# Performance work log

Hardware: AMD Instinct MI355X
Metric: run time of the kernel (lower is better)

## Reference

```python
import jax, jax.numpy as jnp
import numpy as np

B, T, I, H, O, L = 64, 1024, 128, 512, 64, 3


def setup_inputs() -> dict:
    key = jax.random.key(0)
    ks = jax.random.split(key, 16)
    s = 1.0 / np.sqrt(H)  # PyTorch RNN init scale U(-1/sqrt(H), 1/sqrt(H)); use scaled normal
    d = {
        "x": jax.random.normal(ks[0], (B, T, I), jnp.float32),
        "h0": jnp.zeros((L, B, H), jnp.float32),
        "w_ih0": jax.random.normal(ks[1], (H, I), jnp.float32) * s,
        "w_hh0": jax.random.normal(ks[2], (H, H), jnp.float32) * s,
        "b_ih0": jax.random.normal(ks[3], (H,), jnp.float32) * s,
        "b_hh0": jax.random.normal(ks[4], (H,), jnp.float32) * s,
        "w_ih1": jax.random.normal(ks[5], (H, H), jnp.float32) * s,
        "w_hh1": jax.random.normal(ks[6], (H, H), jnp.float32) * s,
        "b_ih1": jax.random.normal(ks[7], (H,), jnp.float32) * s,
        "b_hh1": jax.random.normal(ks[8], (H,), jnp.float32) * s,
        "w_ih2": jax.random.normal(ks[9], (H, H), jnp.float32) * s,
        "w_hh2": jax.random.normal(ks[10], (H, H), jnp.float32) * s,
        "b_ih2": jax.random.normal(ks[11], (H,), jnp.float32) * s,
        "b_hh2": jax.random.normal(ks[12], (H,), jnp.float32) * s,
        "w_fc": jax.random.normal(ks[13], (O, H), jnp.float32) * s,
        "b_fc": jax.random.normal(ks[14], (O,), jnp.float32) * s,
    }
    return d


def _rnn(x, h0, layers):
    # x: [B,T,I]; h0: [L,B,H]; PyTorch: h_t = tanh(x W_ih^T + b_ih + h_{t-1} W_hh^T + b_hh)
    inp = x
    hns = []
    for l, (wi, wh, bi, bh) in enumerate(layers):
        # precompute input projection for all timesteps (one big GEMM), time-major [T,B,H]
        xp = jnp.einsum('bti,hi->tbh', inp, wi) + bi + bh

        def step(h, xt, wh=wh):
            h = jnp.tanh(xt + h @ wh.T)
            return h, h

        hT, ys = jax.lax.scan(step, h0[l], xp)
        hns.append(hT)
        inp = jnp.transpose(ys, (1, 0, 2))  # [B,T,H] feeds next layer
    return inp, jnp.stack(hns)  # [B,T,H], [L,B,H]


def reference(x, h0, w_ih0, w_hh0, b_ih0, b_hh0, w_ih1, w_hh1, b_ih1, b_hh1,
              w_ih2, w_hh2, b_ih2, b_hh2, w_fc, b_fc):
    layers = [(w_ih0, w_hh0, b_ih0, b_hh0),
              (w_ih1, w_hh1, b_ih1, b_hh1),
              (w_ih2, w_hh2, b_ih2, b_hh2)]
    seq, hn = _rnn(x, h0, layers)
    last = seq[:, -1, :]                       # out[:, -1, :]
    out = jax.nn.sigmoid(last @ w_fc.T + b_fc)  # [B,O]
    return out, hn
```

## Files before the change

### kernel.cpp

```cpp
#include <hip/hip_runtime.h>
#include <stdint.h>

#define B_ 64
#define T_ 1024
#define I_ 128
#define H_ 512
#define O_ 64
#define R16 16

typedef __attribute__((ext_vector_type(8))) short bf16x8;
typedef __attribute__((ext_vector_type(4))) float f32x4;
typedef unsigned short u16;
typedef unsigned long long u64;

struct Q2 { u64 a, b; };

__device__ __forceinline__ u16 f2bf(float f) {
  unsigned int u = __builtin_bit_cast(unsigned int, f);
  u += 0x7FFFu + ((u >> 16) & 1u);
  return (u16)(u >> 16);
}
__device__ __forceinline__ float bf2f(u16 h) {
  unsigned int u = ((unsigned int)h) << 16;
  return __builtin_bit_cast(float, u);
}
__device__ __forceinline__ u64 aload(const u64* p) {
  return __hip_atomic_load(p, __ATOMIC_RELAXED, __HIP_MEMORY_SCOPE_AGENT);
}
__device__ __forceinline__ void astore(u64* p, u64 v) {
  __hip_atomic_store(p, v, __ATOMIC_RELAXED, __HIP_MEMORY_SCOPE_AGENT);
}

__global__ void split_kernel(const float* __restrict__ src,
                             u16* __restrict__ hi, u16* __restrict__ lo, int n) {
  int i = blockIdx.x * 256 + threadIdx.x;
  if (i >= n) return;
  float f = src[i];
  u16 h = f2bf(f);
  hi[i] = h;
  lo[i] = f2bf(f - bf2f(h));
}

__global__ void xsplit_kernel(const float* __restrict__ x,
                              u16* __restrict__ hi, u16* __restrict__ lo) {
  int idx = blockIdx.x * 256 + threadIdx.x;
  int i = idx & (I_ - 1);
  int b = (idx >> 7) & (B_ - 1);
  int t = idx >> 13;
  float f = x[(((size_t)b << 10) | t) * I_ + i];
  u16 h = f2bf(f);
  hi[idx] = h;
  lo[idx] = f2bf(f - bf2f(h));
}

__global__ void h0ring_kernel(const float* __restrict__ h0l,
                              u16* __restrict__ hxh, u16* __restrict__ hxl) {
  int idx = blockIdx.x * 256 + threadIdx.x;
  int slot = idx >> 15;
  if (slot == 0) {
    float f = h0l[idx];
    u16 h = f2bf(f);
    hxh[idx] = h;
    hxl[idx] = f2bf(f - bf2f(h));
  } else {
    hxh[idx] = 0x7F80u;
    hxl[idx] = 0x7F80u;
  }
}

__global__ void sentinel_kernel(float* __restrict__ out, float v, int n) {
  int i = blockIdx.x * 256 + threadIdx.x;
  if (i < n) out[i] = v;
}

template <int K, bool ALO>
__global__ __launch_bounds__(256) void proj_gemm(
    const u16* __restrict__ Ahi, const u16* __restrict__ Alo,
    const u16* __restrict__ Whi, const u16* __restrict__ Wlo,
    const float* __restrict__ bih, const float* __restrict__ bhh,
    float* __restrict__ xp) {
  __shared__ u16 lhs[2][128 * 72];
  const int tid = threadIdx.x;
  const int w = tid >> 6, l = tid & 63;
  const int r15 = l & 15, g4 = l >> 4;
  const int Mbase = blockIdx.x * 128;
  const int Nbase = blockIdx.y * 128;
  f32x4 acc[2][8];
#pragma unroll
  for (int bt = 0; bt < 2; ++bt)
#pragma unroll
    for (int ct = 0; ct < 8; ++ct) acc[bt][ct] = (f32x4){0.f, 0.f, 0.f, 0.f};

  for (int kc = 0; kc < K; kc += 64) {
    __syncthreads();
#pragma unroll
    for (int i = 0; i < 4; ++i) {
      int e = i * 256 + tid;
      int c = e >> 3, kg = (e & 7) * 8;
      *(uint4*)&lhs[0][c * 72 + kg] =
          *(const uint4*)(Whi + (size_t)(Nbase + c) * K + kc + kg);
      *(uint4*)&lhs[1][c * 72 + kg] =
          *(const uint4*)(Wlo + (size_t)(Nbase + c) * K + kc + kg);
    }
    __syncthreads();
#pragma unroll
    for (int kt = 0; kt < 2; ++kt) {
      bf16x8 ah[2], al[2];
#pragma unroll
      for (int bt = 0; bt < 2; ++bt) {
        int row = Mbase + w * 32 + bt * 16 + r15;
        int koff = kc + kt * 32 + g4 * 8;
        ah[bt] = *(const bf16x8*)(Ahi + (size_t)row * K + koff);
        if (ALO) al[bt] = *(const bf16x8*)(Alo + (size_t)row * K + koff);
      }
#pragma unroll
      for (int ct = 0; ct < 8; ++ct) {
        int lo_off = (ct * 16 + r15) * 72 + kt * 32 + g4 * 8;
        bf16x8 bh = *(const bf16x8*)&lhs[0][lo_off];
        bf16x8 bl = *(const bf16x8*)&lhs[1][lo_off];
#pragma unroll
        for (int bt = 0; bt < 2; ++bt) {
          acc[bt][ct] = __builtin_amdgcn_mfma_f32_16x16x32_bf16(ah[bt], bh, acc[bt][ct], 0, 0, 0);
          acc[bt][ct] = __builtin_amdgcn_mfma_f32_16x16x32_bf16(ah[bt], bl, acc[bt][ct], 0, 0, 0);
          if (ALO)
            acc[bt][ct] = __builtin_amdgcn_mfma_f32_16x16x32_bf16(al[bt], bh, acc[bt][ct], 0, 0, 0);
        }
      }
    }
  }
#pragma unroll
  for (int ct = 0; ct < 8; ++ct) {
    int col = Nbase + ct * 16 + r15;
    float bc = bih[col] + bhh[col];
#pragma unroll
    for (int bt = 0; bt < 2; ++bt) {
#pragma unroll
      for (int j = 0; j < 4; ++j) {
        int row = Mbase + w * 32 + bt * 16 + g4 * 4 + j;
        xp[(size_t)row * H_ + col] = acc[bt][ct][j] + bc;
      }
    }
  }
}

__global__ __launch_bounds__(128, 1) void scan_kernel(
    const u16* __restrict__ whh_hi, const u16* __restrict__ whh_lo,
    const float* __restrict__ xp,
    u16* __restrict__ yhi,
    u16* __restrict__ hxh, u16* __restrict__ hxl,
    float* __restrict__ hn_out) {
  __shared__ __align__(16) char lds[131072];
  const int tid = threadIdx.x;
  const int l = tid & 63, w = tid >> 6;
  const int bg = blockIdx.x >> 4, sub = blockIdx.x & 15;
  const int r15 = l & 15, g4 = l >> 4;
  const int j0 = (sub * 2 + w) * 16;
  const int bb = bg * 16;
  const int wbase = 65536 + w * 32768;

#pragma unroll
  for (int i = 0; i < 16; ++i) {
    int row = i, cc = l;
    int dst = wbase + row * 1024 + ((cc * 16) ^ ((row & 7) << 4));
    *(uint4*)(lds + dst) = *(const uint4*)(whh_hi + (size_t)(j0 + row) * H_ + cc * 8);
    *(uint4*)(lds + dst + 16384) = *(const uint4*)(whh_lo + (size_t)(j0 + row) * H_ + cc * 8);
  }
  __syncthreads();

  const int sr = tid >> 3, sc = tid & 7;
  const int sxr = (sr & 7) << 4;
  const int rxr = (r15 & 7) << 4;
  const int rdoff = r15 * 1024;

  const float* xpp = xp + (size_t)(bb + r15) * H_ + j0 + g4 * 4;
  f32x4 xpv = *(const f32x4*)xpp;

  for (int t = 0; t < T_; ++t) {
    const int slot = t & (R16 - 1), slot1 = (t + 1) & (R16 - 1);
    const u64* gh = (const u64*)(hxh + ((size_t)slot * B_ + bb + sr) * H_);
    const u64* gl = (const u64*)(hxl + ((size_t)slot * B_ + bb + sr) * H_);
    u64 vh[16], vl[16];
    for (;;) {
#pragma unroll
      for (int i = 0; i < 8; ++i) {
        int u = sc * 2 + i * 16;
        vh[2 * i] = aload(gh + u);
        vh[2 * i + 1] = aload(gh + u + 1);
        vl[2 * i] = aload(gl + u);
        vl[2 * i + 1] = aload(gl + u + 1);
      }
      bool ok = true;
#pragma unroll
      for (int i = 0; i < 16; ++i)
        ok = ok && ((vh[i] >> 48) != 0x7F80ull) && ((vl[i] >> 48) != 0x7F80ull);
      if (ok) break;
      __builtin_amdgcn_s_sleep(1);
    }
    char* base = lds + (t & 1) * 32768;
#pragma unroll
    for (int i = 0; i < 8; ++i) {
      int kb = (sc * 16 + i * 128) ^ sxr;
      *(uint4*)(base + sr * 1024 + kb) = __builtin_bit_cast(uint4, Q2{vh[2 * i], vh[2 * i + 1]});
      *(uint4*)(base + 16384 + sr * 1024 + kb) =
          __builtin_bit_cast(uint4, Q2{vl[2 * i], vl[2 * i + 1]});
    }
    __syncthreads();
    f32x4 a0 = xpv, a1 = {0.f, 0.f, 0.f, 0.f}, a2 = a1, a3 = a1;
#pragma unroll
    for (int kt = 0; kt < 16; ++kt) {
      int kb = (kt * 64 + g4 * 16) ^ rxr;
      bf16x8 hv = *(const bf16x8*)(base + rdoff + kb);
      bf16x8 lv = *(const bf16x8*)(base + 16384 + rdoff + kb);
      bf16x8 wv = *(const bf16x8*)(lds + wbase + rdoff + kb);
      bf16x8 wlv = *(const bf16x8*)(lds + wbase + rdoff + kb + 16384);
      f32x4* ac = (kt & 3) == 0 ? &a0 : (kt & 3) == 1 ? &a1 : (kt & 3) == 2 ? &a2 : &a3;
      *ac = __builtin_amdgcn_mfma_f32_16x16x32_bf16(wv, hv, *ac, 0, 0, 0);
      *ac = __builtin_amdgcn_mfma_f32_16x16x32_bf16(wlv, hv, *ac, 0, 0, 0);
      *ac = __builtin_amdgcn_mfma_f32_16x16x32_bf16(wv, lv, *ac, 0, 0, 0);
    }
    f32x4 s = (a0 + a1) + (a2 + a3);
    float v[4];
#pragma unroll
    for (int j = 0; j < 4; ++j) {
      float e = __expf(2.0f * s[j]);
      v[j] = 1.0f - 2.0f * __builtin_amdgcn_rcpf(e + 1.0f);
    }
    u64 hip = 0, lop = 0;
#pragma unroll
    for (int j = 0; j < 4; ++j) {
      u16 hh = f2bf(v[j]);
      u16 ll = f2bf(v[j] - bf2f(hh));
      hip |= (u64)hh << (16 * j);
      lop |= (u64)ll << (16 * j);
    }
    if (t < T_ - 1) {
      size_t so = ((size_t)slot1 * B_ + bb + r15) * (size_t)H_ + j0 + g4 * 4;
      astore((u64*)hxh + (so >> 2), hip);
      astore((u64*)hxl + (so >> 2), lop);
      const int slotS = (t + 9) & (R16 - 1);
      size_t ss = ((size_t)slotS * B_ + bb + r15) * (size_t)H_ + j0 + g4 * 4;
      astore((u64*)hxh + (ss >> 2), 0x7F807F807F807F80ull);
      astore((u64*)hxl + (ss >> 2), 0x7F807F807F807F80ull);
    }
    *(u64*)(yhi + ((size_t)t * B_ + bb + r15) * H_ + j0 + g4 * 4) = hip;
    if (t == T_ - 1) {
      f32x4 hv4 = {v[0], v[1], v[2], v[3]};
      *(f32x4*)(hn_out + (size_t)(bb + r15) * H_ + j0 + g4 * 4) = hv4;
    } else {
      xpv = *(const f32x4*)(xpp + (size_t)(t + 1) * B_ * H_);
    }
  }
}

__global__ __launch_bounds__(64) void fc_kernel(const float* __restrict__ hn2,
                                                const float* __restrict__ wfc,
                                                const float* __restrict__ bfc,
                                                float* __restrict__ out) {
  int b = blockIdx.x, o = threadIdx.x;
  __shared__ float hs[H_];
  for (int i = o; i < H_; i += 64) hs[i] = hn2[(size_t)b * H_ + i];
  __syncthreads();
  float acc = bfc[o];
#pragma unroll 4
  for (int k = 0; k < H_; k += 4) {
    float4 wv = *(const float4*)(wfc + (size_t)o * H_ + k);
    acc += hs[k] * wv.x + hs[k + 1] * wv.y + hs[k + 2] * wv.z + hs[k + 3] * wv.w;
  }
  out[b * O_ + o] = 1.f / (1.f + expf(-acc));
}

extern "C" void kernel_launch(void* const* d_in, const int* in_sizes, int n_in,
                              void* d_out, int out_size, void* d_ws, size_t ws_size,
                              hipStream_t stream) {
  (void)in_sizes; (void)n_in; (void)out_size;
  const float* x = (const float*)d_in[0];
  const float* h0 = (const float*)d_in[1];
  const float* w_ih[3] = {(const float*)d_in[2], (const float*)d_in[6], (const float*)d_in[10]};
  const float* w_hh[3] = {(const float*)d_in[3], (const float*)d_in[7], (const float*)d_in[11]};
  const float* b_ih[3] = {(const float*)d_in[4], (const float*)d_in[8], (const float*)d_in[12]};
  const float* b_hh[3] = {(const float*)d_in[5], (const float*)d_in[9], (const float*)d_in[13]};
  const float* w_fc = (const float*)d_in[14];
  const float* b_fc = (const float*)d_in[15];
  float* out = (float*)d_out;
  float* hn = out + B_ * O_;

  char* p = (char*)d_ws;
  auto carve = [&](size_t bytes) {
    char* r = p;
    p += (bytes + 255) & ~(size_t)255;
    return r;
  };
  float* xp = (float*)carve((size_t)T_ * B_ * H_ * 4);
  u16* yhi = (u16*)carve((size_t)T_ * B_ * H_ * 2);
  u16* hxh = (u16*)carve((size_t)R16 * B_ * H_ * 2);
  u16* hxl = (u16*)carve((size_t)R16 * B_ * H_ * 2);
  u16 *whhh[3], *whhl[3], *wihh[3], *wihl[3];
  for (int l = 0; l < 3; ++l) {
    whhh[l] = (u16*)carve((size_t)H_ * H_ * 2);
    whhl[l] = (u16*)carve((size_t)H_ * H_ * 2);
    int kin = (l == 0) ? I_ : H_;
    wihh[l] = (u16*)carve((size_t)H_ * kin * 2);
    wihl[l] = (u16*)carve((size_t)H_ * kin * 2);
  }
  size_t required = (size_t)(p - (char*)d_ws);
  if (required > ws_size) {
    int n = B_ * O_ + 3 * B_ * H_;
    sentinel_kernel<<<(n + 255) / 256, 256, 0, stream>>>(out, (float)(ws_size >> 20), n);
    return;
  }
  u16* xhi = yhi;
  u16* xlo = yhi + (size_t)T_ * B_ * I_;

  for (int l = 0; l < 3; ++l) {
    split_kernel<<<H_ * H_ / 256, 256, 0, stream>>>(w_hh[l], whhh[l], whhl[l], H_ * H_);
    int kin = (l == 0) ? I_ : H_;
    split_kernel<<<H_ * kin / 256, 256, 0, stream>>>(w_ih[l], wihh[l], wihl[l], H_ * kin);
  }
  xsplit_kernel<<<T_ * B_ * I_ / 256, 256, 0, stream>>>(x, xhi, xlo);

  for (int l = 0; l < 3; ++l) {
    h0ring_kernel<<<R16 * B_ * H_ / 256, 256, 0, stream>>>(h0 + (size_t)l * B_ * H_, hxh, hxl);
    if (l == 0)
      proj_gemm<I_, true><<<dim3(T_ * B_ / 128, H_ / 128), 256, 0, stream>>>(
          xhi, xlo, wihh[0], wihl[0], b_ih[0], b_hh[0], xp);
    else
      proj_gemm<H_, false><<<dim3(T_ * B_ / 128, H_ / 128), 256, 0, stream>>>(
          yhi, yhi, wihh[l], wihl[l], b_ih[l], b_hh[l], xp);
    scan_kernel<<<64, 128, 0, stream>>>(whhh[l], whhl[l], xp, yhi, hxh, hxl,
                                        hn + (size_t)l * B_ * H_);
  }
  fc_kernel<<<B_, O_, 0, stream>>>(hn + 2 * (size_t)B_ * H_, w_fc, b_fc, out);
}
```

Baseline: 9.230 ms.

## Interleave two batch groups per scan block to hide cross-block sync latency

```diff
diff --git a/kernel.cpp b/kernel.cpp
--- a/kernel.cpp
+++ b/kernel.cpp
@@ -143,6 +143,94 @@
   }
 }
 
+#define ISSUE(S, bb, slot)                                                   \
+  do {                                                                       \
+    const u64* gh_ = (const u64*)(hxh + ((size_t)(slot)*B_ + (bb) + sr) * H_); \
+    const u64* gl_ = (const u64*)(hxl + ((size_t)(slot)*B_ + (bb) + sr) * H_); \
+    _Pragma("unroll") for (int i = 0; i < 8; ++i) {                          \
+      int u_ = sc * 2 + i * 16;                                              \
+      vh##S[2 * i] = aload(gh_ + u_);                                        \
+      vh##S[2 * i + 1] = aload(gh_ + u_ + 1);                                \
+      vl##S[2 * i] = aload(gl_ + u_);                                        \
+      vl##S[2 * i + 1] = aload(gl_ + u_ + 1);                                \
+    }                                                                        \
+  } while (0)
+
+#define SPIN(S, bb, slot)                                                    \
+  do {                                                                       \
+    for (;;) {                                                               \
+      bool ok_ = true;                                                       \
+      _Pragma("unroll") for (int i = 0; i < 16; ++i) ok_ =                   \
+          ok_ && ((vh##S[i] >> 48) != 0x7F80ull) &&                          \
+          ((vl##S[i] >> 48) != 0x7F80ull);                                   \
+      if (ok_) break;                                                        \
+      __builtin_amdgcn_s_sleep(1);                                           \
+      ISSUE(S, bb, slot);                                                    \
+    }                                                                        \
+  } while (0)
+
+#define STAGE(S, bufoff)                                                     \
+  do {                                                                       \
+    char* sb_ = lds + (bufoff);                                              \
+    _Pragma("unroll") for (int i = 0; i < 8; ++i) {                          \
+      int kb_ = (sc * 16 + i * 128) ^ sxr;                                   \
+      *(uint4*)(sb_ + sr * 1024 + kb_) =                                     \
+          __builtin_bit_cast(uint4, Q2{vh##S[2 * i], vh##S[2 * i + 1]});     \
+      *(uint4*)(sb_ + 16384 + sr * 1024 + kb_) =                             \
+          __builtin_bit_cast(uint4, Q2{vl##S[2 * i], vl##S[2 * i + 1]});     \
+    }                                                                        \
+  } while (0)
+
+#define COMPUTE(bufoff, bb, xpv, xpp, t)                                     \
+  do {                                                                       \
+    char* cb_ = lds + (bufoff);                                              \
+    f32x4 a0_ = (xpv), a1_ = {0.f, 0.f, 0.f, 0.f}, a2_ = a1_, a3_ = a1_;     \
+    _Pragma("unroll") for (int kt = 0; kt < 16; ++kt) {                      \
+      int kb_ = (kt * 64 + g4 * 16) ^ rxr;                                   \
+      bf16x8 hv_ = *(const bf16x8*)(cb_ + rdoff + kb_);                      \
+      bf16x8 lv_ = *(const bf16x8*)(cb_ + 16384 + rdoff + kb_);              \
+      bf16x8 wv_ = *(const bf16x8*)(lds + wbase + rdoff + kb_);              \
+      bf16x8 wl_ = *(const bf16x8*)(lds + wbase + rdoff + kb_ + 16384);      \
+      f32x4* ac_ = (kt & 3) == 0   ? &a0_                                    \
+                   : (kt & 3) == 1 ? &a1_                                    \
+                   : (kt & 3) == 2 ? &a2_                                    \
+                                   : &a3_;                                   \
+      *ac_ = __builtin_amdgcn_mfma_f32_16x16x32_bf16(wv_, hv_, *ac_, 0, 0, 0); \
+      *ac_ = __builtin_amdgcn_mfma_f32_16x16x32_bf16(wl_, hv_, *ac_, 0, 0, 0); \
+      *ac_ = __builtin_amdgcn_mfma_f32_16x16x32_bf16(wv_, lv_, *ac_, 0, 0, 0); \
+    }                                                                        \
+    f32x4 s_ = (a0_ + a1_) + (a2_ + a3_);                                    \
+    float v_[4];                                                             \
+    _Pragma("unroll") for (int j = 0; j < 4; ++j) {                          \
+      float e_ = __expf(2.0f * s_[j]);                                       \
+      v_[j] = 1.0f - 2.0f * __builtin_amdgcn_rcpf(e_ + 1.0f);                \
+    }                                                                        \
+    u64 hip_ = 0, lop_ = 0;                                                  \
+    _Pragma("unroll") for (int j = 0; j < 4; ++j) {                          \
+      u16 hh_ = f2bf(v_[j]);                                                 \
+      u16 ll_ = f2bf(v_[j] - bf2f(hh_));                                     \
+      hip_ |= (u64)hh_ << (16 * j);                                          \
+      lop_ |= (u64)ll_ << (16 * j);                                          \
+    }                                                                        \
+    if ((t) < T_ - 1) {                                                      \
+      size_t so_ =                                                           \
+          ((size_t)(((t) + 1) & 15) * B_ + (bb) + r15) * (size_t)H_ + j0 + g4 * 4; \
+      astore((u64*)hxh + (so_ >> 2), hip_);                                  \
+      astore((u64*)hxl + (so_ >> 2), lop_);                                  \
+      size_t ss_ =                                                           \
+          ((size_t)(((t) + 9) & 15) * B_ + (bb) + r15) * (size_t)H_ + j0 + g4 * 4; \
+      astore((u64*)hxh + (ss_ >> 2), 0x7F807F807F807F80ull);                 \
+      astore((u64*)hxl + (ss_ >> 2), 0x7F807F807F807F80ull);                 \
+    }                                                                        \
+    *(u64*)(yhi + ((size_t)(t)*B_ + (bb) + r15) * H_ + j0 + g4 * 4) = hip_;  \
+    if ((t) == T_ - 1) {                                                     \
+      f32x4 hv4_ = {v_[0], v_[1], v_[2], v_[3]};                             \
+      *(f32x4*)(hn_out + (size_t)((bb) + r15) * H_ + j0 + g4 * 4) = hv4_;    \
+    } else {                                                                 \
+      (xpv) = *(const f32x4*)((xpp) + (size_t)((t) + 1) * B_ * H_);          \
+    }                                                                        \
+  } while (0)
+
 __global__ __launch_bounds__(128, 1) void scan_kernel(
     const u16* __restrict__ whh_hi, const u16* __restrict__ whh_lo,
     const float* __restrict__ xp,
@@ -152,10 +240,10 @@
   __shared__ __align__(16) char lds[131072];
   const int tid = threadIdx.x;
   const int l = tid & 63, w = tid >> 6;
-  const int bg = blockIdx.x >> 4, sub = blockIdx.x & 15;
+  const int pair = blockIdx.x >> 4, sub = blockIdx.x & 15;
   const int r15 = l & 15, g4 = l >> 4;
   const int j0 = (sub * 2 + w) * 16;
-  const int bb = bg * 16;
+  const int bbA = pair * 32, bbB = bbA + 16;
   const int wbase = 65536 + w * 32768;
 
 #pragma unroll
@@ -172,83 +260,30 @@
   const int rxr = (r15 & 7) << 4;
   const int rdoff = r15 * 1024;
 
-  const float* xpp = xp + (size_t)(bb + r15) * H_ + j0 + g4 * 4;
-  f32x4 xpv = *(const f32x4*)xpp;
+  const float* xppA = xp + (size_t)(bbA + r15) * H_ + j0 + g4 * 4;
+  const float* xppB = xp + (size_t)(bbB + r15) * H_ + j0 + g4 * 4;
+  f32x4 xpvA = *(const f32x4*)xppA;
+  f32x4 xpvB = *(const f32x4*)xppB;
+
+  u64 vhA[16], vlA[16], vhB[16], vlB[16];
+  ISSUE(A, bbA, 0);
 
   for (int t = 0; t < T_; ++t) {
-    const int slot = t & (R16 - 1), slot1 = (t + 1) & (R16 - 1);
-    const u64* gh = (const u64*)(hxh + ((size_t)slot * B_ + bb + sr) * H_);
-    const u64* gl = (const u64*)(hxl + ((size_t)slot * B_ + bb + sr) * H_);
-    u64 vh[16], vl[16];
-    for (;;) {
-#pragma unroll
-      for (int i = 0; i < 8; ++i) {
-        int u = sc * 2 + i * 16;
-        vh[2 * i] = aload(gh + u);
-        vh[2 * i + 1] = aload(gh + u + 1);
-        vl[2 * i] = aload(gl + u);
-        vl[2 * i + 1] = aload(gl + u + 1);
-      }
-      bool ok = true;
-#pragma unroll
-      for (int i = 0; i < 16; ++i)
-        ok = ok && ((vh[i] >> 48) != 0x7F80ull) && ((vl[i] >> 48) != 0x7F80ull);
-      if (ok) break;
-      __builtin_amdgcn_s_sleep(1);
+    const int slot = t & 15;
+    SPIN(A, bbA, slot);
+    ISSUE(B, bbB, slot);
+    __builtin_amdgcn_sched_barrier(0);
+    STAGE(A, 0);
+    __syncthreads();
+    COMPUTE(0, bbA, xpvA, xppA, t);
+    SPIN(B, bbB, slot);
+    if (t < T_ - 1) {
+      ISSUE(A, bbA, (t + 1) & 15);
+      __builtin_amdgcn_sched_barrier(0);
     }
-    char* base = lds + (t & 1) * 32768;
-#pragma unroll
-    for (int i = 0; i < 8; ++i) {
-      int kb = (sc * 16 + i * 128) ^ sxr;
-      *(uint4*)(base + sr * 1024 + kb) = __builtin_bit_cast(uint4, Q2{vh[2 * i], vh[2 * i + 1]});
-      *(uint4*)(base + 16384 + sr * 1024 + kb) =
-          __builtin_bit_cast(uint4, Q2{vl[2 * i], vl[2 * i + 1]});
-    }
+    STAGE(B, 32768);
     __syncthreads();
-    f32x4 a0 = xpv, a1 = {0.f, 0.f, 0.f, 0.f}, a2 = a1, a3 = a1;
-#pragma unroll
-    for (int kt = 0; kt < 16; ++kt) {
-      int kb = (kt * 64 + g4 * 16) ^ rxr;
-      bf16x8 hv = *(const bf16x8*)(base + rdoff + kb);
-      bf16x8 lv = *(const bf16x8*)(base + 16384 + rdoff + kb);
-      bf16x8 wv = *(const bf16x8*)(lds + wbase + rdoff + kb);
-      bf16x8 wlv = *(const bf16x8*)(lds + wbase + rdoff + kb + 16384);
-      f32x4* ac = (kt & 3) == 0 ? &a0 : (kt & 3) == 1 ? &a1 : (kt & 3) == 2 ? &a2 : &a3;
-      *ac = __builtin_amdgcn_mfma_f32_16x16x32_bf16(wv, hv, *ac, 0, 0, 0);
-      *ac = __builtin_amdgcn_mfma_f32_16x16x32_bf16(wlv, hv, *ac, 0, 0, 0);
-      *ac = __builtin_amdgcn_mfma_f32_16x16x32_bf16(wv, lv, *ac, 0, 0, 0);
-    }
-    f32x4 s = (a0 + a1) + (a2 + a3);
-    float v[4];
-#pragma unroll
-    for (int j = 0; j < 4; ++j) {
-      float e = __expf(2.0f * s[j]);
-      v[j] = 1.0f - 2.0f * __builtin_amdgcn_rcpf(e + 1.0f);
-    }
-    u64 hip = 0, lop = 0;
-#pragma unroll
-    for (int j = 0; j < 4; ++j) {
-      u16 hh = f2bf(v[j]);
-      u16 ll = f2bf(v[j] - bf2f(hh));
-      hip |= (u64)hh << (16 * j);
-      lop |= (u64)ll << (16 * j);
-    }
-    if (t < T_ - 1) {
-      size_t so = ((size_t)slot1 * B_ + bb + r15) * (size_t)H_ + j0 + g4 * 4;
-      astore((u64*)hxh + (so >> 2), hip);
-      astore((u64*)hxl + (so >> 2), lop);
-      const int slotS = (t + 9) & (R16 - 1);
-      size_t ss = ((size_t)slotS * B_ + bb + r15) * (size_t)H_ + j0 + g4 * 4;
-      astore((u64*)hxh + (ss >> 2), 0x7F807F807F807F80ull);
-      astore((u64*)hxl + (ss >> 2), 0x7F807F807F807F80ull);
-    }
-    *(u64*)(yhi + ((size_t)t * B_ + bb + r15) * H_ + j0 + g4 * 4) = hip;
-    if (t == T_ - 1) {
-      f32x4 hv4 = {v[0], v[1], v[2], v[3]};
-      *(f32x4*)(hn_out + (size_t)(bb + r15) * H_ + j0 + g4 * 4) = hv4;
-    } else {
-      xpv = *(const f32x4*)(xpp + (size_t)(t + 1) * B_ * H_);
-    }
+    COMPUTE(32768, bbB, xpvB, xppB, t);
   }
 }
 
@@ -326,7 +361,7 @@
     else
       proj_gemm<H_, false><<<dim3(T_ * B_ / 128, H_ / 128), 256, 0, stream>>>(
           yhi, yhi, wihh[l], wihl[l], b_ih[l], b_hh[l], xp);
-    scan_kernel<<<64, 128, 0, stream>>>(whhh[l], whhl[l], xp, yhi, hxh, hxl,
+    scan_kernel<<<32, 128, 0, stream>>>(whhh[l], whhl[l], xp, yhi, hxh, hxl,
                                         hn + (size_t)l * B_ * H_);
   }
   fc_kernel<<<B_, O_, 0, stream>>>(hn + 2 * (size_t)B_ * H_, w_fc, b_fc, out);
```

Result: slower. 17.52 ms (+89.8%).
